# Kernel tuning notes

Measured on AMD Instinct MI355X. Metric: run time of the kernel, lower is better.

## Reference

```python
import jax, jax.numpy as jnp
import numpy as np

N_ATOM = 4096
NHEADS = 8
C_PER_HEAD = 64
BLOCK_SIZE = 128
LOCAL_WINDOW = 512


def setup_inputs() -> dict:
    key = jax.random.key(0)
    k1, k2, k3, k4 = jax.random.split(key, 4)
    q = jax.random.normal(k1, (N_ATOM, NHEADS, C_PER_HEAD), dtype=jnp.float32)
    k = jax.random.normal(k2, (N_ATOM, NHEADS, C_PER_HEAD), dtype=jnp.float32)
    v = jax.random.normal(k3, (N_ATOM, NHEADS, C_PER_HEAD), dtype=jnp.float32)
    pair_bias = jax.random.normal(k4, (N_ATOM, N_ATOM, NHEADS), dtype=jnp.float32)
    return {"q": q, "k": k, "v": v, "pair_bias": pair_bias}


def reference(q, k, v, pair_bias):
    # Local block-sparse attention: banded blockmask with blocks_per_side
    # = max(1, local_window // block_size) blocks on each side of the diagonal.
    # NOTE: pair_bias is accepted by the original forward but never used
    # (it is not passed to block_sparse_attn_func), so it is ignored here.
    N, H, D = q.shape
    B = BLOCK_SIZE
    bps = max(1, LOCAL_WINDOW // BLOCK_SIZE)  # blocks per side = 4
    nrow = N // B  # N is a multiple of block_size here
    scale = jnp.asarray(D, q.dtype) ** -0.5  # softmax_scale=None -> 1/sqrt(d)

    qb = q.reshape(nrow, B, H, D)
    kb = k.reshape(nrow, B, H, D)
    vb = v.reshape(nrow, B, H, D)

    offs = jnp.arange(-bps, bps + 1)                      # [W], W = 2*bps+1
    cols = jnp.arange(nrow)[:, None] + offs[None, :]      # [nrow, W]
    valid = (cols >= 0) & (cols < nrow)                   # band edge mask
    colsc = jnp.clip(cols, 0, nrow - 1)

    kg = kb[colsc]  # [nrow, W, B, H, D] -- only band blocks gathered
    vg = vb[colsc]

    # scores: [nrow, H, B, W, B]
    scores = jnp.einsum('rihd,rwjhd->rhiwj', qb, kg) * scale
    neg_inf = jnp.asarray(-jnp.inf, scores.dtype)
    scores = jnp.where(valid[:, None, None, :, None], scores, neg_inf)

    p = jax.nn.softmax(scores.reshape(nrow, H, B, -1), axis=-1)
    p = p.reshape(scores.shape)

    out = jnp.einsum('rhiwj,rwjhd->rihd', p, vg)  # [nrow, B, H, D]
    return out.reshape(N, H, D)
```

## Files before the change

### kernel.cpp

```cpp
#include <hip/hip_runtime.h>
#include <hip/hip_bf16.h>

#define NATOM 4096
#define NH 8
#define DIMD 64
#define BLK 128
#define NROW 32
#define BPS 4
#define ROWSTRIDE (NH * DIMD)
#define SCALE 0.125f
#define L2E 1.4426950408889634f

#define TILE_EL (BLK * DIMD)
#define V_LD 136
#define P_LD 136
#define K_LDF 72
#define RED_ST 68

#define HEAD_ELEMS (NATOM * DIMD)
#define WS_NEEDED  (2u * NH * HEAD_ELEMS * 2u)

typedef __attribute__((ext_vector_type(8))) short bf16x8;
typedef __attribute__((ext_vector_type(4))) float f32x4;
typedef __attribute__((ext_vector_type(4))) unsigned int u32x4;

__device__ __forceinline__ short f2bf(float x) {
    unsigned int u = __builtin_bit_cast(unsigned int, x);
    unsigned int r = (u + 0x7fffu + ((u >> 16) & 1u)) >> 16;
    return (short)r;
}
__device__ __forceinline__ unsigned int cvtpk(float lo, float hi) {
    unsigned int r;
    asm("v_cvt_pk_bf16_f32 %0, %1, %2" : "=v"(r) : "v"(lo), "v"(hi));
    return r;
}
__device__ __forceinline__ void drain_gll() {
    asm volatile("s_waitcnt vmcnt(0)" ::: "memory");
}

extern "C" __global__ __launch_bounds__(256)
void prep_kernel(const float* __restrict__ k, const float* __restrict__ v,
                 short* __restrict__ Kb, short* __restrict__ Vt)
{
    __shared__ short Tr[DIMD * V_LD];
    const int bid  = blockIdx.x;
    const int h    = bid & 7;
    const int part = bid >> 3;
    const int t    = threadIdx.x;

    if (part < 32) {
        const int nb = part;
        #pragma unroll
        for (int i = 0; i < 4; ++i) {
            int idx = i * 256 + t;
            int row = idx >> 3;
            int c   = idx & 7;
            int d0  = c * 8;
            int grow = nb * BLK + row;
            const float* src = k + (size_t)grow * ROWSTRIDE + h * DIMD + d0;
            float4 a = *(const float4*)src;
            float4 cc = *(const float4*)(src + 4);
            bf16x8 f;
            f[0] = f2bf(a.x); f[1] = f2bf(a.y); f[2] = f2bf(a.z); f[3] = f2bf(a.w);
            f[4] = f2bf(cc.x); f[5] = f2bf(cc.y); f[6] = f2bf(cc.z); f[7] = f2bf(cc.w);
            *(bf16x8*)(Kb + (size_t)h * HEAD_ELEMS + (size_t)grow * DIMD
                       + ((c ^ (grow & 7)) * 8)) = f;
        }
    } else {
        const int nb = part - 32;
        const int vd = t & 63;
        const int g  = t >> 6;
        const float* vp = v + (size_t)(nb * BLK) * ROWSTRIDE + h * DIMD + vd;
        #pragma unroll
        for (int i = 0; i < 8; ++i) {
            int n4 = i * 16 + g * 4;
            const float* vr = vp + (size_t)n4 * ROWSTRIDE;
            short4 s4;
            s4.x = f2bf(vr[0 * ROWSTRIDE]);
            s4.y = f2bf(vr[1 * ROWSTRIDE]);
            s4.z = f2bf(vr[2 * ROWSTRIDE]);
            s4.w = f2bf(vr[3 * ROWSTRIDE]);
            *(short4*)&Tr[vd * V_LD + n4] = s4;
        }
        __syncthreads();
        #pragma unroll
        for (int i = 0; i < 4; ++i) {
            int s  = i * 256 + t;
            int d  = s >> 4;
            int cc = s & 15;
            int kc = cc >> 2;
            int l2 = cc & 3;
            int kA = kc * 32 + l2 * 4;
            short4 a  = *(const short4*)&Tr[d * V_LD + kA];
            short4 c4 = *(const short4*)&Tr[d * V_LD + kA + 16];
            bf16x8 f;
            f[0] = a.x;  f[1] = a.y;  f[2] = a.z;  f[3] = a.w;
            f[4] = c4.x; f[5] = c4.y; f[6] = c4.z; f[7] = c4.w;
            *(bf16x8*)(Vt + (size_t)h * HEAD_ELEMS + (size_t)nb * TILE_EL
                       + d * BLK + ((cc ^ (d & 15)) * 8)) = f;
        }
    }
}

extern "C" __global__ __launch_bounds__(256, 2)
void bsattn_main(const float* __restrict__ q,
                 const short* __restrict__ Kb,
                 const short* __restrict__ Vt,
                 float* __restrict__ out)
{
    __shared__ __align__(16) char SMEM[4 * 64 * RED_ST * 4 + 256 * 4];
    short* Ksh0 = (short*)SMEM;
    short* Vsh0 = (short*)(SMEM + 32768);
    float* Ored = (float*)SMEM;
    float* Lred = (float*)(SMEM + 4 * 64 * RED_ST * 4);

    const int bid = blockIdx.x;
    const int h   = bid & 7;
    const int br  = bid >> 3;
    const int r   = br >> 1;
    const int t   = threadIdx.x;
    const int w   = t >> 6;
    const int lane = t & 63;
    const int lr = lane >> 4;
    const int lc = lane & 15;

    const int qbase = br * 64;
    bf16x8 qf[4][2];
    #pragma unroll
    for (int qg = 0; qg < 4; ++qg) {
        const float* qp = q + (size_t)(qbase + qg * 16 + lc) * ROWSTRIDE + h * DIMD + lr * 8;
        #pragma unroll
        for (int kc = 0; kc < 2; ++kc) {
            float4 a = *(const float4*)(qp + kc * 32);
            float4 b = *(const float4*)(qp + kc * 32 + 4);
            bf16x8 f;
            f[0] = f2bf(a.x * (SCALE * L2E)); f[1] = f2bf(a.y * (SCALE * L2E));
            f[2] = f2bf(a.z * (SCALE * L2E)); f[3] = f2bf(a.w * (SCALE * L2E));
            f[4] = f2bf(b.x * (SCALE * L2E)); f[5] = f2bf(b.y * (SCALE * L2E));
            f[6] = f2bf(b.z * (SCALE * L2E)); f[7] = f2bf(b.w * (SCALE * L2E));
            qf[qg][kc] = f;
        }
    }
    bf16x8 onesA;
    #pragma unroll
    for (int i = 0; i < 8; ++i) onesA[i] = (short)0x3F80;

    const short* kbase = Kb + (size_t)h * HEAD_ELEMS;
    const short* vbase = Vt + (size_t)h * HEAD_ELEMS;

    f32x4 o[4][4] = {};
    f32x4 lacc[4] = {};

    const int kb0 = (r - BPS > 0) ? (r - BPS) : 0;
    const int kb1 = (r + BPS < NROW - 1) ? (r + BPS) : (NROW - 1);

    const short* kt = kbase + (size_t)kb0 * TILE_EL;
    const short* vt = vbase + (size_t)kb0 * TILE_EL;

#define ISSUE(buf, off)                                                           \
    {                                                                             \
        const short* kq = kt + (size_t)(off) * TILE_EL;                           \
        const short* vq = vt + (size_t)(off) * TILE_EL;                           \
        _Pragma("unroll")                                                         \
        for (int i = 0; i < 4; ++i) {                                             \
            int idx = i * 256 + t;                                                \
            __builtin_amdgcn_global_load_lds(                                     \
                (const __attribute__((address_space(1))) unsigned int*)(kq + idx * 8), \
                (__attribute__((address_space(3))) unsigned int*)(Ksh0 + (buf) * TILE_EL + idx * 8), \
                16, 0, 0);                                                        \
            __builtin_amdgcn_global_load_lds(                                     \
                (const __attribute__((address_space(1))) unsigned int*)(vq + idx * 8), \
                (__attribute__((address_space(3))) unsigned int*)(Vsh0 + (buf) * TILE_EL + idx * 8), \
                16, 0, 0);                                                        \
        }                                                                         \
    }

    ISSUE(0, 0);
    if (kb0 < kb1) ISSUE(1, 1);
    drain_gll();
    __syncthreads();

    int cur = 0;
    for (int kb = kb0; kb <= kb1; ++kb) {
        const short* ks = Ksh0 + cur * TILE_EL;
        const short* vs = Vsh0 + cur * TILE_EL;

        bf16x8 kf[2][2];
        #pragma unroll
        for (int lm = 0; lm < 2; ++lm) {
            int row = w * 32 + lm * 16 + lc;
            #pragma unroll
            for (int kc = 0; kc < 2; ++kc)
                kf[lm][kc] = *(const bf16x8*)&ks[row * DIMD + (((kc * 4 + lr) ^ (row & 7)) * 8)];
        }

        f32x4 s[4][2];
        __builtin_amdgcn_s_setprio(1);
        #pragma unroll
        for (int qg = 0; qg < 4; ++qg) {
            #pragma unroll
            for (int lm = 0; lm < 2; ++lm) {
                f32x4 z = {};
                #pragma unroll
                for (int kc = 0; kc < 2; ++kc)
                    z = __builtin_amdgcn_mfma_f32_16x16x32_bf16(kf[lm][kc], qf[qg][kc], z, 0, 0, 0);
                s[qg][lm] = z;
            }
        }
        __builtin_amdgcn_s_setprio(0);

        #pragma unroll
        for (int qg = 0; qg < 4; ++qg)
            #pragma unroll
            for (int lm = 0; lm < 2; ++lm)
                #pragma unroll
                for (int e = 0; e < 4; ++e)
                    s[qg][lm][e] = __builtin_amdgcn_exp2f(s[qg][lm][e]);

        bf16x8 pf[4];
        #pragma unroll
        for (int qg = 0; qg < 4; ++qg) {
            u32x4 pk;
            pk[0] = cvtpk(s[qg][0][0], s[qg][0][1]);
            pk[1] = cvtpk(s[qg][0][2], s[qg][0][3]);
            pk[2] = cvtpk(s[qg][1][0], s[qg][1][1]);
            pk[3] = cvtpk(s[qg][1][2], s[qg][1][3]);
            pf[qg] = __builtin_bit_cast(bf16x8, pk);
        }

        bf16x8 vf[4];
        #pragma unroll
        for (int dn = 0; dn < 4; ++dn) {
            int d = dn * 16 + lc;
            vf[dn] = *(const bf16x8*)&vs[d * BLK + (((w * 4 + lr) ^ (d & 15)) * 8)];
        }
        __builtin_amdgcn_s_setprio(1);
        #pragma unroll
        for (int qg = 0; qg < 4; ++qg) {
            #pragma unroll
            for (int dn = 0; dn < 4; ++dn)
                o[qg][dn] = __builtin_amdgcn_mfma_f32_16x16x32_bf16(vf[dn], pf[qg], o[qg][dn], 0, 0, 0);
            lacc[qg] = __builtin_amdgcn_mfma_f32_16x16x32_bf16(onesA, pf[qg], lacc[qg], 0, 0, 0);
        }
        __builtin_amdgcn_s_setprio(0);

        drain_gll();
        __syncthreads();
        if (kb + 2 <= kb1) ISSUE(cur, kb - kb0 + 2);
        cur ^= 1;
    }

    #pragma unroll
    for (int qg = 0; qg < 4; ++qg) {
        #pragma unroll
        for (int dn = 0; dn < 4; ++dn) {
            *(f32x4*)&Ored[(w * 64 + qg * 16 + lc) * RED_ST + dn * 16 + lr * 4] = o[qg][dn];
        }
    }
    if (lr == 0) {
        #pragma unroll
        for (int qg = 0; qg < 4; ++qg)
            Lred[w * 64 + qg * 16 + lc] = lacc[qg][0];
    }
    __syncthreads();

    float l = 0.0f;
    #pragma unroll
    for (int wv = 0; wv < 4; ++wv) l += Lred[wv * 64 + w * 16 + lc];
    float inv = 1.0f / l;
    float* orow = out + (size_t)(qbase + w * 16 + lc) * ROWSTRIDE + h * DIMD;
    #pragma unroll
    for (int e4 = 0; e4 < 4; ++e4) {
        f32x4 sum = {};
        #pragma unroll
        for (int wv = 0; wv < 4; ++wv)
            sum += *(const f32x4*)&Ored[(wv * 64 + w * 16 + lc) * RED_ST + lr * 16 + e4 * 4];
        f32x4 rv;
        rv[0] = sum[0] * inv; rv[1] = sum[1] * inv;
        rv[2] = sum[2] * inv; rv[3] = sum[3] * inv;
        *(float4*)(orow + lr * 16 + e4 * 4) = *(float4*)&rv;
    }
#undef ISSUE
}

extern "C" __global__ __launch_bounds__(512)
void bsattn_fallback(const float* __restrict__ q,
                     const float* __restrict__ k,
                     const float* __restrict__ v,
                     float* __restrict__ out)
{
    __shared__ short Ksh[BLK * K_LDF];
    __shared__ short Vsh[DIMD * V_LD];
    __shared__ short Psh[8][16 * P_LD];

    const int r = blockIdx.x;
    const int h = blockIdx.y;
    const int t = threadIdx.x;
    const int w = t >> 6;
    const int lane = t & 63;
    const int lr = lane >> 4;
    const int lc = lane & 15;

    const int krow = t >> 4;
    const int kcol = (t & 15) * 4;
    const int vd  = t & 63;
    const int vkg = t >> 6;

    const int qrow_l = w * 16 + lc;
    const float* qp = q + (size_t)(r * BLK + qrow_l) * ROWSTRIDE + h * DIMD + lr * 8;
    bf16x8 qf[2];
    #pragma unroll
    for (int kc = 0; kc < 2; ++kc) {
        float4 a = *(const float4*)(qp + kc * 32);
        float4 b = *(const float4*)(qp + kc * 32 + 4);
        bf16x8 f;
        f[0] = f2bf(a.x); f[1] = f2bf(a.y); f[2] = f2bf(a.z); f[3] = f2bf(a.w);
        f[4] = f2bf(b.x); f[5] = f2bf(b.y); f[6] = f2bf(b.z); f[7] = f2bf(b.w);
        qf[kc] = f;
    }

    f32x4 acc[4] = {};
    float m_run[4], l_run[4];
    #pragma unroll
    for (int i = 0; i < 4; ++i) { m_run[i] = -1e30f; l_run[i] = 0.0f; }

    const int kb0 = (r - BPS > 0) ? (r - BPS) : 0;
    const int kb1 = (r + BPS < NROW - 1) ? (r + BPS) : (NROW - 1);

    for (int kb = kb0; kb <= kb1; ++kb) {
        __syncthreads();
        const float* kp = k + (size_t)(kb * BLK) * ROWSTRIDE + h * DIMD;
        const float* vp = v + (size_t)(kb * BLK) * ROWSTRIDE + h * DIMD;

        #pragma unroll
        for (int i = 0; i < 4; ++i) {
            float4 kv = *(const float4*)(kp + (size_t)(i * 32 + krow) * ROWSTRIDE + kcol);
            short4 ks;
            ks.x = f2bf(kv.x); ks.y = f2bf(kv.y); ks.z = f2bf(kv.z); ks.w = f2bf(kv.w);
            *(short4*)&Ksh[(i * 32 + krow) * K_LDF + kcol] = ks;

            const float* vr = vp + (size_t)(i * 32 + vkg * 4) * ROWSTRIDE + vd;
            short4 vs;
            vs.x = f2bf(vr[0 * ROWSTRIDE]);
            vs.y = f2bf(vr[1 * ROWSTRIDE]);
            vs.z = f2bf(vr[2 * ROWSTRIDE]);
            vs.w = f2bf(vr[3 * ROWSTRIDE]);
            *(short4*)&Vsh[vd * V_LD + i * 32 + vkg * 4] = vs;
        }
        __syncthreads();

        f32x4 s[8];
        #pragma unroll
        for (int n = 0; n < 8; ++n) {
            f32x4 z = {};
            #pragma unroll
            for (int kc = 0; kc < 2; ++kc) {
                bf16x8 kf = *(const bf16x8*)&Ksh[(n * 16 + lc) * K_LDF + kc * 32 + lr * 8];
                z = __builtin_amdgcn_mfma_f32_16x16x32_bf16(qf[kc], kf, z, 0, 0, 0);
            }
            s[n] = z * SCALE;
        }

        #pragma unroll
        for (int rr = 0; rr < 4; ++rr) {
            float mx = s[0][rr];
            #pragma unroll
            for (int n = 1; n < 8; ++n) mx = fmaxf(mx, s[n][rr]);
            #pragma unroll
            for (int off = 1; off < 16; off <<= 1)
                mx = fmaxf(mx, __shfl_xor(mx, off, 64));
            float mnew = fmaxf(m_run[rr], mx);
            float al = exp2f((m_run[rr] - mnew) * L2E);
            m_run[rr] = mnew;
            float sum = 0.0f;
            #pragma unroll
            for (int n = 0; n < 8; ++n) {
                float p = exp2f((s[n][rr] - mnew) * L2E);
                s[n][rr] = p;
                sum += p;
            }
            #pragma unroll
            for (int off = 1; off < 16; off <<= 1)
                sum += __shfl_xor(sum, off, 64);
            l_run[rr] = l_run[rr] * al + sum;
            #pragma unroll
            for (int dn = 0; dn < 4; ++dn) acc[dn][rr] *= al;
        }

        short* pw = &Psh[w][0];
        #pragma unroll
        for (int n = 0; n < 8; ++n) {
            #pragma unroll
            for (int rr = 0; rr < 4; ++rr) {
                pw[(lr * 4 + rr) * P_LD + n * 16 + lc] = f2bf(s[n][rr]);
            }
        }

        #pragma unroll
        for (int dn = 0; dn < 4; ++dn) {
            f32x4 o = acc[dn];
            #pragma unroll
            for (int kc = 0; kc < 4; ++kc) {
                bf16x8 pfr = *(const bf16x8*)&pw[lc * P_LD + kc * 32 + lr * 8];
                bf16x8 vf = *(const bf16x8*)&Vsh[(dn * 16 + lc) * V_LD + kc * 32 + lr * 8];
                o = __builtin_amdgcn_mfma_f32_16x16x32_bf16(pfr, vf, o, 0, 0, 0);
            }
            acc[dn] = o;
        }
    }

    float* op = out + (size_t)(r * BLK + w * 16) * ROWSTRIDE + h * DIMD;
    #pragma unroll
    for (int rr = 0; rr < 4; ++rr) {
        float inv = 1.0f / l_run[rr];
        float* orow = op + (size_t)(lr * 4 + rr) * ROWSTRIDE;
        #pragma unroll
        for (int dn = 0; dn < 4; ++dn) {
            orow[dn * 16 + lc] = acc[dn][rr] * inv;
        }
    }
}

extern "C" void kernel_launch(void* const* d_in, const int* in_sizes, int n_in,
                              void* d_out, int out_size, void* d_ws, size_t ws_size,
                              hipStream_t stream) {
    const float* q = (const float*)d_in[0];
    const float* k = (const float*)d_in[1];
    const float* v = (const float*)d_in[2];
    float* out = (float*)d_out;

    if (ws_size >= (size_t)WS_NEEDED) {
        short* Kb = (short*)d_ws;
        short* Vt = Kb + (size_t)NH * HEAD_ELEMS;
        prep_kernel<<<512, 256, 0, stream>>>(k, v, Kb, Vt);
        bsattn_main<<<512, 256, 0, stream>>>(q, Kb, Vt, out);
    } else {
        bsattn_fallback<<<dim3(NROW, NH), 512, 0, stream>>>(q, k, v, out);
    }
}
```

Before: 27.97 us.

## Load K/V fragments directly from global into registers, dropping LDS staging

Replaces the LDS double-buffered global_load_lds pipeline with direct per-wave global loads of K and V fragments into registers, prefetching the next tile into a second register set while computing the current one. The prep kernel drops the XOR swizzle, since no LDS bank conflicts remain to avoid. This removes the per-tile barriers and waitcnt drains. In exchange each wave fetches from global/L2 without shared reuse, using narrower loads, and register pressure rises from the doubled fragment sets.

New measurement: 35.21 us. 25.9% more time.

```diff
diff --git a/kernel.cpp b/kernel.cpp
--- a/kernel.cpp
+++ b/kernel.cpp
@@ -34,9 +34,6 @@
     asm("v_cvt_pk_bf16_f32 %0, %1, %2" : "=v"(r) : "v"(lo), "v"(hi));
     return r;
 }
-__device__ __forceinline__ void drain_gll() {
-    asm volatile("s_waitcnt vmcnt(0)" ::: "memory");
-}
 
 extern "C" __global__ __launch_bounds__(256)
 void prep_kernel(const float* __restrict__ k, const float* __restrict__ v,
@@ -54,8 +51,7 @@
         for (int i = 0; i < 4; ++i) {
             int idx = i * 256 + t;
             int row = idx >> 3;
-            int c   = idx & 7;
-            int d0  = c * 8;
+            int d0  = (idx & 7) * 8;
             int grow = nb * BLK + row;
             const float* src = k + (size_t)grow * ROWSTRIDE + h * DIMD + d0;
             float4 a = *(const float4*)src;
@@ -63,8 +59,7 @@
             bf16x8 f;
             f[0] = f2bf(a.x); f[1] = f2bf(a.y); f[2] = f2bf(a.z); f[3] = f2bf(a.w);
             f[4] = f2bf(cc.x); f[5] = f2bf(cc.y); f[6] = f2bf(cc.z); f[7] = f2bf(cc.w);
-            *(bf16x8*)(Kb + (size_t)h * HEAD_ELEMS + (size_t)grow * DIMD
-                       + ((c ^ (grow & 7)) * 8)) = f;
+            *(bf16x8*)(Kb + (size_t)h * HEAD_ELEMS + (size_t)grow * DIMD + d0) = f;
         }
     } else {
         const int nb = part - 32;
@@ -97,7 +92,7 @@
             f[0] = a.x;  f[1] = a.y;  f[2] = a.z;  f[3] = a.w;
             f[4] = c4.x; f[5] = c4.y; f[6] = c4.z; f[7] = c4.w;
             *(bf16x8*)(Vt + (size_t)h * HEAD_ELEMS + (size_t)nb * TILE_EL
-                       + d * BLK + ((cc ^ (d & 15)) * 8)) = f;
+                       + d * BLK + cc * 8) = f;
         }
     }
 }
@@ -109,8 +104,6 @@
                  float* __restrict__ out)
 {
     __shared__ __align__(16) char SMEM[4 * 64 * RED_ST * 4 + 256 * 4];
-    short* Ksh0 = (short*)SMEM;
-    short* Vsh0 = (short*)(SMEM + 32768);
     float* Ored = (float*)SMEM;
     float* Lred = (float*)(SMEM + 4 * 64 * RED_ST * 4);
 
@@ -154,100 +147,74 @@
     const int kb0 = (r - BPS > 0) ? (r - BPS) : 0;
     const int kb1 = (r + BPS < NROW - 1) ? (r + BPS) : (NROW - 1);
 
-    const short* kt = kbase + (size_t)kb0 * TILE_EL;
-    const short* vt = vbase + (size_t)kb0 * TILE_EL;
-
-#define ISSUE(buf, off)                                                           \
+    bf16x8 kfA[2][2], vfA[4], kfB[2][2], vfB[4];
+
+#define LOADT(kf, vf, kb_)                                                        \
     {                                                                             \
-        const short* kq = kt + (size_t)(off) * TILE_EL;                           \
-        const short* vq = vt + (size_t)(off) * TILE_EL;                           \
-        _Pragma("unroll")                                                         \
-        for (int i = 0; i < 4; ++i) {                                             \
-            int idx = i * 256 + t;                                                \
-            __builtin_amdgcn_global_load_lds(                                     \
-                (const __attribute__((address_space(1))) unsigned int*)(kq + idx * 8), \
-                (__attribute__((address_space(3))) unsigned int*)(Ksh0 + (buf) * TILE_EL + idx * 8), \
-                16, 0, 0);                                                        \
-            __builtin_amdgcn_global_load_lds(                                     \
-                (const __attribute__((address_space(1))) unsigned int*)(vq + idx * 8), \
-                (__attribute__((address_space(3))) unsigned int*)(Vsh0 + (buf) * TILE_EL + idx * 8), \
-                16, 0, 0);                                                        \
+        const short* kt_ = kbase + (size_t)(kb_) * TILE_EL;                       \
+        const short* vt_ = vbase + (size_t)(kb_) * TILE_EL;                       \
+        _Pragma("unroll")                                                         \
+        for (int lm = 0; lm < 2; ++lm)                                            \
+            _Pragma("unroll")                                                     \
+            for (int kc = 0; kc < 2; ++kc)                                        \
+                kf[lm][kc] = *(const bf16x8*)(kt_ + (w * 32 + lm * 16 + lc) * DIMD \
+                                              + kc * 32 + lr * 8);                \
+        _Pragma("unroll")                                                         \
+        for (int dn = 0; dn < 4; ++dn)                                            \
+            vf[dn] = *(const bf16x8*)(vt_ + (dn * 16 + lc) * BLK + w * 32 + lr * 8); \
+    }
+
+#define COMPUTE(kf, vf)                                                           \
+    {                                                                             \
+        f32x4 s[4][2];                                                            \
+        __builtin_amdgcn_s_setprio(1);                                            \
+        _Pragma("unroll")                                                         \
+        for (int qg = 0; qg < 4; ++qg) {                                          \
+            _Pragma("unroll")                                                     \
+            for (int lm = 0; lm < 2; ++lm) {                                      \
+                f32x4 z = {};                                                     \
+                z = __builtin_amdgcn_mfma_f32_16x16x32_bf16(kf[lm][0], qf[qg][0], z, 0, 0, 0); \
+                z = __builtin_amdgcn_mfma_f32_16x16x32_bf16(kf[lm][1], qf[qg][1], z, 0, 0, 0); \
+                s[qg][lm] = z;                                                    \
+            }                                                                     \
         }                                                                         \
-    }
-
-    ISSUE(0, 0);
-    if (kb0 < kb1) ISSUE(1, 1);
-    drain_gll();
-    __syncthreads();
-
-    int cur = 0;
-    for (int kb = kb0; kb <= kb1; ++kb) {
-        const short* ks = Ksh0 + cur * TILE_EL;
-        const short* vs = Vsh0 + cur * TILE_EL;
-
-        bf16x8 kf[2][2];
-        #pragma unroll
-        for (int lm = 0; lm < 2; ++lm) {
-            int row = w * 32 + lm * 16 + lc;
-            #pragma unroll
-            for (int kc = 0; kc < 2; ++kc)
-                kf[lm][kc] = *(const bf16x8*)&ks[row * DIMD + (((kc * 4 + lr) ^ (row & 7)) * 8)];
-        }
-
-        f32x4 s[4][2];
-        __builtin_amdgcn_s_setprio(1);
-        #pragma unroll
-        for (int qg = 0; qg < 4; ++qg) {
-            #pragma unroll
-            for (int lm = 0; lm < 2; ++lm) {
-                f32x4 z = {};
-                #pragma unroll
-                for (int kc = 0; kc < 2; ++kc)
-                    z = __builtin_amdgcn_mfma_f32_16x16x32_bf16(kf[lm][kc], qf[qg][kc], z, 0, 0, 0);
-                s[qg][lm] = z;
-            }
-        }
-        __builtin_amdgcn_s_setprio(0);
-
-        #pragma unroll
-        for (int qg = 0; qg < 4; ++qg)
-            #pragma unroll
-            for (int lm = 0; lm < 2; ++lm)
-                #pragma unroll
-                for (int e = 0; e < 4; ++e)
-                    s[qg][lm][e] = __builtin_amdgcn_exp2f(s[qg][lm][e]);
-
-        bf16x8 pf[4];
-        #pragma unroll
-        for (int qg = 0; qg < 4; ++qg) {
-            u32x4 pk;
-            pk[0] = cvtpk(s[qg][0][0], s[qg][0][1]);
-            pk[1] = cvtpk(s[qg][0][2], s[qg][0][3]);
-            pk[2] = cvtpk(s[qg][1][0], s[qg][1][1]);
-            pk[3] = cvtpk(s[qg][1][2], s[qg][1][3]);
-            pf[qg] = __builtin_bit_cast(bf16x8, pk);
-        }
-
-        bf16x8 vf[4];
-        #pragma unroll
-        for (int dn = 0; dn < 4; ++dn) {
-            int d = dn * 16 + lc;
-            vf[dn] = *(const bf16x8*)&vs[d * BLK + (((w * 4 + lr) ^ (d & 15)) * 8)];
-        }
-        __builtin_amdgcn_s_setprio(1);
-        #pragma unroll
-        for (int qg = 0; qg < 4; ++qg) {
-            #pragma unroll
-            for (int dn = 0; dn < 4; ++dn)
-                o[qg][dn] = __builtin_amdgcn_mfma_f32_16x16x32_bf16(vf[dn], pf[qg], o[qg][dn], 0, 0, 0);
-            lacc[qg] = __builtin_amdgcn_mfma_f32_16x16x32_bf16(onesA, pf[qg], lacc[qg], 0, 0, 0);
-        }
-        __builtin_amdgcn_s_setprio(0);
-
-        drain_gll();
-        __syncthreads();
-        if (kb + 2 <= kb1) ISSUE(cur, kb - kb0 + 2);
-        cur ^= 1;
+        __builtin_amdgcn_s_setprio(0);                                            \
+        _Pragma("unroll")                                                         \
+        for (int qg = 0; qg < 4; ++qg)                                            \
+            _Pragma("unroll")                                                     \
+            for (int lm = 0; lm < 2; ++lm)                                        \
+                _Pragma("unroll")                                                 \
+                for (int e = 0; e < 4; ++e)                                       \
+                    s[qg][lm][e] = __builtin_amdgcn_exp2f(s[qg][lm][e]);          \
+        bf16x8 pf[4];                                                             \
+        _Pragma("unroll")                                                         \
+        for (int qg = 0; qg < 4; ++qg) {                                          \
+            u32x4 pk;                                                             \
+            pk[0] = cvtpk(s[qg][0][0], s[qg][0][1]);                              \
+            pk[1] = cvtpk(s[qg][0][2], s[qg][0][3]);                              \
+            pk[2] = cvtpk(s[qg][1][0], s[qg][1][1]);                              \
+            pk[3] = cvtpk(s[qg][1][2], s[qg][1][3]);                              \
+            pf[qg] = __builtin_bit_cast(bf16x8, pk);                              \
+        }                                                                         \
+        __builtin_amdgcn_s_setprio(1);                                            \
+        _Pragma("unroll")                                                         \
+        for (int qg = 0; qg < 4; ++qg) {                                          \
+            _Pragma("unroll")                                                     \
+            for (int dn = 0; dn < 4; ++dn)                                        \
+                o[qg][dn] = __builtin_amdgcn_mfma_f32_16x16x32_bf16(vf[dn], pf[qg], o[qg][dn], 0, 0, 0); \
+            lacc[qg] = __builtin_amdgcn_mfma_f32_16x16x32_bf16(onesA, pf[qg], lacc[qg], 0, 0, 0); \
+        }                                                                         \
+        __builtin_amdgcn_s_setprio(0);                                            \
+    }
+
+    LOADT(kfA, vfA, kb0);
+    for (int kb = kb0; kb <= kb1; kb += 2) {
+        if (kb + 1 <= kb1) LOADT(kfB, vfB, kb + 1);
+        COMPUTE(kfA, vfA);
+        if (kb + 1 <= kb1) {
+            if (kb + 2 <= kb1) LOADT(kfA, vfA, kb + 2);
+            COMPUTE(kfB, vfB);
+        }
     }
 
     #pragma unroll
@@ -280,7 +247,8 @@
         rv[2] = sum[2] * inv; rv[3] = sum[3] * inv;
         *(float4*)(orow + lr * 16 + e4 * 4) = *(float4*)&rv;
     }
-#undef ISSUE
+#undef LOADT
+#undef COMPUTE
 }
 
 extern "C" __global__ __launch_bounds__(512)
```
